# Performance work log

Measured on AMD Instinct MI355X. Metric: run time of the kernel, lower is better.

## Reference

```python
import jax, jax.numpy as jnp
import numpy as np

IN_DIM = 128
OUT_DIM = 128
NUM_HEADS = 8
HEAD_DIM = OUT_DIM // NUM_HEADS  # 16
FFN_DIM = OUT_DIM * 2
LN_EPS = 1e-5


def _layer_norm(x, g, b):
    mu = jnp.mean(x, axis=-1, keepdims=True)
    var = jnp.var(x, axis=-1, keepdims=True)
    return (x - mu) * jax.lax.rsqrt(var + LN_EPS) * g + b


def setup_inputs() -> dict:
    key = jax.random.key(0)
    ks = jax.random.split(key, 12)
    B, N = 4, 2048
    s_in = 1.0 / np.sqrt(IN_DIM)
    s_out = 1.0 / np.sqrt(OUT_DIM)
    s_ffn = 1.0 / np.sqrt(FFN_DIM)
    return {
        "adj_matrix": jax.random.randint(ks[0], (N, N), 0, 2, dtype=jnp.int32),
        "h": jax.random.normal(ks[1], (B, N, IN_DIM), dtype=jnp.float32),
        # Q/K/V: Linear(in_dim, out_dim) with use_bias=False, stored as [in, out]
        "Wq": jax.random.uniform(ks[2], (IN_DIM, OUT_DIM), jnp.float32, -s_in, s_in),
        "Wk": jax.random.uniform(ks[3], (IN_DIM, OUT_DIM), jnp.float32, -s_in, s_in),
        "Wv": jax.random.uniform(ks[4], (IN_DIM, OUT_DIM), jnp.float32, -s_in, s_in),
        "Wo": jax.random.uniform(ks[5], (OUT_DIM, OUT_DIM), jnp.float32, -s_out, s_out),
        "bo": jnp.zeros((OUT_DIM,), jnp.float32),
        "ln1_g": jnp.ones((OUT_DIM,), jnp.float32),
        "ln1_b": jnp.zeros((OUT_DIM,), jnp.float32),
        "W1": jax.random.uniform(ks[6], (OUT_DIM, FFN_DIM), jnp.float32, -s_out, s_out),
        "b1": jnp.zeros((FFN_DIM,), jnp.float32),
        "W2": jax.random.uniform(ks[7], (FFN_DIM, OUT_DIM), jnp.float32, -s_ffn, s_ffn),
        "b2": jnp.zeros((OUT_DIM,), jnp.float32),
        "ln2_g": jnp.ones((OUT_DIM,), jnp.float32),
        "ln2_b": jnp.zeros((OUT_DIM,), jnp.float32),
    }


def reference(adj_matrix, h, Wq, Wk, Wv, Wo, bo, ln1_g, ln1_b,
              W1, b1, W2, b2, ln2_g, ln2_b):
    B, N, _ = h.shape
    # QKV projections -> [B, N, H, D]
    Q = (h @ Wq).reshape(B, N, NUM_HEADS, HEAD_DIM)
    K = (h @ Wk).reshape(B, N, NUM_HEADS, HEAD_DIM)
    V = (h @ Wv).reshape(B, N, NUM_HEADS, HEAD_DIM)
    scores = jnp.einsum('bnhd,bmhd->bhnm', Q, K) / jnp.sqrt(
        jnp.asarray(HEAD_DIM, jnp.float32))
    # adjacency-masked attention: mask broadcast over batch and heads
    mask = (adj_matrix == 0)[None, None, :, :]  # [1,1,N,N]
    scores = jnp.where(mask, -jnp.inf, scores)
    attn = jax.nn.softmax(scores, axis=-1)
    attn_out = jnp.einsum('bhnm,bmhd->bnhd', attn, V).reshape(B, N, OUT_DIM)
    # output projection + residual + LN
    x = h + (attn_out @ Wo + bo)
    x = _layer_norm(x, ln1_g, ln1_b)
    # FFN + residual + LN
    y = jax.nn.relu(x @ W1 + b1) @ W2 + b2
    x = _layer_norm(x + y, ln2_g, ln2_b)
    return x
```

## Files before the change

kernel.cpp:

```cpp
#include <hip/hip_runtime.h>

#define B_   4
#define N_   2048
#define DIM  128
#define NH   8
#define HD   16
#define FFN_ 256
#define LN_EPS 1e-5f
#define BN   (B_*N_)
#define LOG2E 1.44269504f

#if __has_builtin(__builtin_amdgcn_exp2f)
#define EXP2(x) __builtin_amdgcn_exp2f(x)
#else
#define EXP2(x) exp2f(x)
#endif

typedef __bf16 bf16x8 __attribute__((ext_vector_type(8)));
typedef short  s16x8  __attribute__((ext_vector_type(8)));
typedef float  f32x16 __attribute__((ext_vector_type(16)));
typedef unsigned int u32x4 __attribute__((ext_vector_type(4)));

template<class T> struct as_short_vec { using type = s16x8; };

template <class T>
__device__ auto mfma_try(T a, T b, f32x16 c, int)
    -> decltype(__builtin_amdgcn_mfma_f32_32x32x16_bf16(a, b, c, 0, 0, 0)) {
  return __builtin_amdgcn_mfma_f32_32x32x16_bf16(a, b, c, 0, 0, 0);
}
template <class T>
__device__ f32x16 mfma_try(T a, T b, f32x16 c, long) {
  return __builtin_amdgcn_mfma_f32_32x32x16_bf16(
      __builtin_bit_cast(typename as_short_vec<T>::type, a),
      __builtin_bit_cast(typename as_short_vec<T>::type, b), c, 0, 0, 0);
}
__device__ __forceinline__ f32x16 mfma_bf(bf16x8 a, bf16x8 b, f32x16 c) {
  return mfma_try(a, b, c, 0);
}

__global__ __launch_bounds__(256) void k_prep(
    const int* __restrict__ adj,
    const float* __restrict__ W1, const float* __restrict__ W2,
    const float* __restrict__ Wq, const float* __restrict__ Wk,
    const float* __restrict__ Wv, const float* __restrict__ Wo,
    unsigned int* __restrict__ adjbT,
    __bf16* __restrict__ W1t, __bf16* __restrict__ W2t,
    __bf16* __restrict__ Wqt, __bf16* __restrict__ Wkt,
    __bf16* __restrict__ Wvt, __bf16* __restrict__ Wot,
    __bf16* __restrict__ onesb) {
    const int blk = blockIdx.x;
    const int tid = threadIdx.x;
    if (blk < 16384) {
        long long idx = (long long)blk * 256 + tid;
        int v = adj[idx] != 0;
        unsigned long long m = __ballot(v);
        if ((tid & 63) == 0) {
            int q  = (int)(idx >> 11);
            int kc = ((int)idx & 2047) >> 5;
            adjbT[(size_t)kc * 2048 + q]       = (unsigned)m;
            adjbT[(size_t)(kc + 1) * 2048 + q] = (unsigned)(m >> 32);
        }
    } else {
        const int g = (blk - 16384) * 256 + tid;
        {
            int k = g >> 8, n = g & 255;
            W1t[(size_t)n * 128 + k] = (__bf16)W1[(size_t)k * 256 + n];
        }
        {
            int k = g >> 7, n = g & 127;
            W2t[(size_t)n * 256 + k] = (__bf16)W2[(size_t)k * 128 + n];
        }
        if (g < 16384) {
            int k = g >> 7, n = g & 127;
            size_t s = (size_t)k * 128 + n, d = (size_t)n * 128 + k;
            Wqt[d] = (__bf16)(Wq[s] * (0.25f * LOG2E));
            Wkt[d] = (__bf16)Wk[s];
            Wvt[d] = (__bf16)Wv[s];
            Wot[d] = (__bf16)Wo[s];
        }
        if (g < 2080) onesb[g] = (__bf16)1.0f;
    }
}

__global__ __launch_bounds__(768) void k_qkv(
    const float* __restrict__ h,
    const __bf16* __restrict__ Wqt, const __bf16* __restrict__ Wkt,
    const __bf16* __restrict__ Wvt,
    __bf16* __restrict__ Qb, __bf16* __restrict__ Kb, __bf16* __restrict__ Vt) {
    const int r0   = blockIdx.x * 32;
    const int tid  = threadIdx.x;
    const int w    = tid >> 6;
    const int mat  = w >> 2;
    const int ct   = w & 3;
    const int lane = tid & 63;
    const int l31  = lane & 31, hi = lane >> 5;

    __shared__ __bf16 Hs[32 * 128];

    if (tid < 512) {
        int row = tid >> 4, u = tid & 15;
        const float* src = h + (size_t)(r0 + row) * DIM + u * 8;
        float4 f0 = *(const float4*)src, f1 = *(const float4*)(src + 4);
        bf16x8 v;
        v[0] = (__bf16)f0.x; v[1] = (__bf16)f0.y; v[2] = (__bf16)f0.z; v[3] = (__bf16)f0.w;
        v[4] = (__bf16)f1.x; v[5] = (__bf16)f1.y; v[6] = (__bf16)f1.z; v[7] = (__bf16)f1.w;
        int byte = (row * 256 + u * 16) ^ ((row & 7) << 4);
        *(bf16x8*)((char*)Hs + byte) = v;
    }
    __syncthreads();

    const __bf16* Wsel = (mat == 0) ? Wqt : ((mat == 1) ? Wkt : Wvt);

    f32x16 a;
    #pragma unroll
    for (int i = 0; i < 16; ++i) a[i] = 0.f;
    #pragma unroll
    for (int kk = 0; kk < 8; ++kk) {
        int byte = (l31 * 256 + kk * 32 + hi * 16) ^ ((l31 & 7) << 4);
        bf16x8 af = *(const bf16x8*)((const char*)Hs + byte);
        a = mfma_bf(af, *(const bf16x8*)(Wsel + (size_t)(ct * 32 + l31) * 128 + kk * 16 + hi * 8), a);
    }

    const int n  = ct * 32 + l31;
    const int hh = n >> 4, d = n & 15;
    const int b  = r0 >> 11;
    const int nloc0 = r0 & (N_ - 1);
    if (mat < 2) {
        __bf16* dst = (mat == 0) ? Qb : Kb;
        const size_t qbase = (size_t)(b * NH + hh) * N_;
        #pragma unroll
        for (int r = 0; r < 16; ++r) {
            int mm = (r & 3) + 8 * (r >> 2) + 4 * hi;
            dst[(qbase + nloc0 + mm) * HD + d] = (__bf16)a[r];
        }
    } else {
        const size_t vbase = ((size_t)(b * NH + hh) * HD + d) * N_;
        #pragma unroll
        for (int r = 0; r < 16; ++r) {
            int mm   = (r & 3) + 8 * (r >> 2) + 4 * hi;
            int nloc = nloc0 + mm;
            int gg = (nloc >> 2) & 7;
            int ng = (gg & 4) | ((gg & 1) << 1) | ((gg >> 1) & 1);
            Vt[vbase + ((nloc & ~31) | (ng << 2) | (nloc & 3))] = (__bf16)a[r];
        }
    }
}

__global__ __launch_bounds__(512, 4) void k_attn(
    const __bf16* __restrict__ Qb, const __bf16* __restrict__ Kb,
    const __bf16* __restrict__ Vt, const unsigned int* __restrict__ adjbT,
    const __bf16* __restrict__ onesb,
    __bf16* __restrict__ AOb) {
    const int bid  = (blockIdx.x & 7) * 256 + (blockIdx.x >> 3);
    const int qt   = bid & 63;
    const int hh   = (bid >> 6) & 7;
    const int b    = bid >> 9;
    const int kq   = threadIdx.x >> 6;
    const int lane = threadIdx.x & 63;
    const int l31  = lane & 31, hi = lane >> 5;
    const int q     = qt * 32 + l31;
    const int kbase = kq * 256;
    const int NT    = 8;

    __shared__ float accL[7][64][9];
    __shared__ uint2 lutM[16];

    if (threadIdx.x < 16) {
        unsigned v = threadIdx.x;
        lutM[v].x = ((v & 1u) ? 0xFFFFu : 0u) | ((v & 2u) ? 0xFFFF0000u : 0u);
        lutM[v].y = ((v & 4u) ? 0xFFFFu : 0u) | ((v & 8u) ? 0xFFFF0000u : 0u);
    }
    __syncthreads();

    const __bf16* Qh = Qb + (size_t)(b * NH + hh) * N_ * HD;
    const __bf16* Kp = Kb + (size_t)(b * NH + hh) * N_ * HD
                          + (size_t)(kbase + l31) * HD + hi * 8;
    const __bf16* Vp = ((l31 < 16)
        ? (Vt + ((size_t)(b * NH + hh) * HD + l31) * N_)
        : onesb) + kbase + hi * 8;
    const unsigned int* wp = adjbT + (size_t)(kq * NT) * 2048 + q;

    bf16x8 qf = *(const bf16x8*)(Qh + (size_t)q * HD + hi * 8);

    f32x16 acc;
    #pragma unroll
    for (int i = 0; i < 16; ++i) acc[i] = 0.f;
    const f32x16 z = {};

    bf16x8 kf  = *(const bf16x8*)Kp;
    bf16x8 vfa = *(const bf16x8*)Vp;
    bf16x8 vfb = *(const bf16x8*)(Vp + 16);
    unsigned int w32 = wp[0];

    #pragma unroll
    for (int t = 0; t < NT; ++t) {
        bf16x8 kf_n = {}, vfa_n = {}, vfb_n = {};
        unsigned int w32_n = 0;
        if (t + 1 < NT) {
            kf_n  = *(const bf16x8*)(Kp + (t + 1) * 32 * HD);
            vfa_n = *(const bf16x8*)(Vp + (t + 1) * 32);
            vfb_n = *(const bf16x8*)(Vp + (t + 1) * 32 + 16);
            w32_n = wp[(size_t)(t + 1) * 2048];
        }

        const unsigned ws = w32 >> (4 * hi);
        uint2 e0 = lutM[ws & 15u];
        uint2 e1 = lutM[(ws >> 8) & 15u];
        uint2 e2 = lutM[(ws >> 16) & 15u];
        uint2 e3 = lutM[(ws >> 24) & 15u];

        f32x16 st = mfma_bf(kf, qf, z);

        float p[16];
        #pragma unroll
        for (int r = 0; r < 16; ++r) p[r] = EXP2(st[r]);
        bf16x8 pa, pb;
        #pragma unroll
        for (int r = 0; r < 8; ++r) { pa[r] = (__bf16)p[r]; pb[r] = (__bf16)p[r + 8]; }

        u32x4 mA = {e0.x, e0.y, e1.x, e1.y};
        u32x4 mB = {e2.x, e2.y, e3.x, e3.y};
        pa = __builtin_bit_cast(bf16x8, __builtin_bit_cast(u32x4, pa) & mA);
        pb = __builtin_bit_cast(bf16x8, __builtin_bit_cast(u32x4, pb) & mB);

        acc = mfma_bf(vfa, pa, acc);
        acc = mfma_bf(vfb, pb, acc);

        if (t + 1 < NT) { kf = kf_n; vfa = vfa_n; vfb = vfb_n; w32 = w32_n; }
    }

    if (kq != 0) {
        #pragma unroll
        for (int r = 0; r < 9; ++r) accL[kq - 1][lane][r] = acc[r];
    }
    __syncthreads();
    if (kq == 0) {
        float tot[9];
        #pragma unroll
        for (int r = 0; r < 9; ++r) {
            float v = acc[r];
            #pragma unroll
            for (int i = 0; i < 7; ++i) v += accL[i][lane][r];
            tot[r] = v;
        }
        float inv = 1.f / tot[8];
        bf16x8 ov;
        #pragma unroll
        for (int r = 0; r < 8; ++r) ov[r] = (__bf16)(tot[r] * inv);
        u32x4 ou = __builtin_bit_cast(u32x4, ov);
        __bf16* op = AOb + ((size_t)(b * N_ + q)) * DIM + hh * HD + 4 * hi;
        uint2 w0 = { ou[0], ou[1] }, w1 = { ou[2], ou[3] };
        *(uint2*)op       = w0;
        *(uint2*)(op + 8) = w1;
    }
}

__global__ __launch_bounds__(512) void k_tail(
    const __bf16* __restrict__ AOb, const float* __restrict__ h,
    const __bf16* __restrict__ Wot, const float* __restrict__ bo,
    const float* __restrict__ g1, const float* __restrict__ b1ln,
    const __bf16* __restrict__ W1t, const float* __restrict__ b1,
    const __bf16* __restrict__ W2t, const float* __restrict__ b2,
    const float* __restrict__ g2, const float* __restrict__ b2ln,
    float* __restrict__ out) {
    const int r0   = blockIdx.x * 32;
    const int tid  = threadIdx.x;
    const int w    = tid >> 6;
    const int ct   = w & 3;
    const int kh   = w >> 2;
    const int lane = tid & 63;
    const int l31  = lane & 31, hi = lane >> 5;

    __shared__ __bf16 As[32 * 128];
    __shared__ __bf16 Xs[32 * 128];
    __shared__ __bf16 Ts[32 * 256];
    __shared__ float  vv[32][DIM];
    __shared__ float  accT[4][64][16];

    {
        int row = tid >> 4, u = tid & 15;
        bf16x8 v = *(const bf16x8*)(AOb + (size_t)(r0 + row) * DIM + u * 8);
        int byte = (row * 256 + u * 16) ^ ((row & 7) << 4);
        *(bf16x8*)((char*)As + byte) = v;
    }
    __syncthreads();

    f32x16 acc;
    #pragma unroll
    for (int i = 0; i < 16; ++i) acc[i] = 0.f;
    #pragma unroll
    for (int kk = 0; kk < 4; ++kk) {
        int kkk = kh * 4 + kk;
        int byte = (l31 * 256 + kkk * 32 + hi * 16) ^ ((l31 & 7) << 4);
        bf16x8 a = *(const bf16x8*)((const char*)As + byte);
        acc = mfma_bf(a, *(const bf16x8*)(Wot + (size_t)(ct * 32 + l31) * 128 + kkk * 16 + hi * 8), acc);
    }
    if (kh == 1) {
        #pragma unroll
        for (int r = 0; r < 16; ++r) accT[ct][lane][r] = acc[r];
    }
    __syncthreads();
    if (kh == 0) {
        int n = ct * 32 + l31;
        float bb = bo[n];
        #pragma unroll
        for (int r = 0; r < 16; ++r) {
            int mm = (r & 3) + 8 * (r >> 2) + 4 * hi;
            vv[mm][n] = acc[r] + accT[ct][lane][r] + bb + h[(size_t)(r0 + mm) * DIM + n];
        }
    }
    __syncthreads();

    {
        const int ln = lane;
        float gc0 = g1[ln], bc0 = b1ln[ln], gc1 = g1[ln + 64], bc1 = b1ln[ln + 64];
        #pragma unroll
        for (int i = 0; i < 4; ++i) {
            int rr = w * 4 + i;
            float x0 = vv[rr][ln], x1 = vv[rr][ln + 64];
            float s = x0 + x1, s2 = x0 * x0 + x1 * x1;
            for (int off = 1; off < 64; off <<= 1) {
                s  += __shfl_xor(s,  off);
                s2 += __shfl_xor(s2, off);
            }
            float mu  = s * (1.f / DIM);
            float var = s2 * (1.f / DIM) - mu * mu;
            float rs  = rsqrtf(var + LN_EPS);
            int byte0 = (rr * 256 + ln * 2) ^ ((rr & 7) << 4);
            int byte1 = (rr * 256 + (ln + 64) * 2) ^ ((rr & 7) << 4);
            *(__bf16*)((char*)Xs + byte0) = (__bf16)((x0 - mu) * rs * gc0 + bc0);
            *(__bf16*)((char*)Xs + byte1) = (__bf16)((x1 - mu) * rs * gc1 + bc1);
        }
    }
    __syncthreads();

    f32x16 acc1;
    #pragma unroll
    for (int i = 0; i < 16; ++i) acc1[i] = 0.f;
    #pragma unroll
    for (int kk = 0; kk < 8; ++kk) {
        int byte = (l31 * 256 + kk * 32 + hi * 16) ^ ((l31 & 7) << 4);
        bf16x8 a = *(const bf16x8*)((const char*)Xs + byte);
        acc1 = mfma_bf(a, *(const bf16x8*)(W1t + (size_t)(w * 32 + l31) * 128 + kk * 16 + hi * 8), acc1);
    }
    {
        int n = w * 32 + l31;
        float bb = b1[n];
        #pragma unroll
        for (int r = 0; r < 16; ++r) {
            int mm = (r & 3) + 8 * (r >> 2) + 4 * hi;
            float v = fmaxf(acc1[r] + bb, 0.f);
            int byte = (mm * 512 + n * 2) ^ ((mm & 7) << 4);
            *(__bf16*)((char*)Ts + byte) = (__bf16)v;
        }
    }
    __syncthreads();

    f32x16 acc2;
    #pragma unroll
    for (int i = 0; i < 16; ++i) acc2[i] = 0.f;
    #pragma unroll
    for (int kk = 0; kk < 8; ++kk) {
        int kkk = kh * 8 + kk;
        int byte = (l31 * 512 + kkk * 32 + hi * 16) ^ ((l31 & 7) << 4);
        bf16x8 a = *(const bf16x8*)((const char*)Ts + byte);
        acc2 = mfma_bf(a, *(const bf16x8*)(W2t + (size_t)(ct * 32 + l31) * 256 + kkk * 16 + hi * 8), acc2);
    }
    if (kh == 1) {
        #pragma unroll
        for (int r = 0; r < 16; ++r) accT[ct][lane][r] = acc2[r];
    }
    __syncthreads();
    if (kh == 0) {
        int n = ct * 32 + l31;
        float bb = b2[n];
        #pragma unroll
        for (int r = 0; r < 16; ++r) {
            int mm = (r & 3) + 8 * (r >> 2) + 4 * hi;
            int byteR = (mm * 256 + n * 2) ^ ((mm & 7) << 4);
            float resid = (float)*(const __bf16*)((const char*)Xs + byteR);
            vv[mm][n] = acc2[r] + accT[ct][lane][r] + bb + resid;
        }
    }
    __syncthreads();

    {
        const int ln = lane;
        float gc0 = g2[ln], bc0 = b2ln[ln], gc1 = g2[ln + 64], bc1 = b2ln[ln + 64];
        #pragma unroll
        for (int i = 0; i < 4; ++i) {
            int rr = w * 4 + i;
            float x0 = vv[rr][ln], x1 = vv[rr][ln + 64];
            float s = x0 + x1, s2 = x0 * x0 + x1 * x1;
            for (int off = 1; off < 64; off <<= 1) {
                s  += __shfl_xor(s,  off);
                s2 += __shfl_xor(s2, off);
            }
            float mu  = s * (1.f / DIM);
            float var = s2 * (1.f / DIM) - mu * mu;
            float rs  = rsqrtf(var + LN_EPS);
            size_t o = (size_t)(r0 + rr) * DIM;
            out[o + ln]      = (x0 - mu) * rs * gc0 + bc0;
            out[o + ln + 64] = (x1 - mu) * rs * gc1 + bc1;
        }
    }
}

extern "C" void kernel_launch(void* const* d_in, const int* in_sizes, int n_in,
                              void* d_out, int out_size, void* d_ws, size_t ws_size,
                              hipStream_t stream) {
    const int*   adj = (const int*)  d_in[0];
    const float* h   = (const float*)d_in[1];
    const float* Wq  = (const float*)d_in[2];
    const float* Wk  = (const float*)d_in[3];
    const float* Wv  = (const float*)d_in[4];
    const float* Wo  = (const float*)d_in[5];
    const float* bo  = (const float*)d_in[6];
    const float* g1  = (const float*)d_in[7];
    const float* b1l = (const float*)d_in[8];
    const float* W1  = (const float*)d_in[9];
    const float* b1  = (const float*)d_in[10];
    const float* W2  = (const float*)d_in[11];
    const float* b2  = (const float*)d_in[12];
    const float* g2  = (const float*)d_in[13];
    const float* b2l = (const float*)d_in[14];
    float* out = (float*)d_out;

    __bf16* AOb = (__bf16*)d_ws;
    unsigned int* adjbT = (unsigned int*)(AOb + (size_t)BN * DIM);
    __bf16* Qb  = (__bf16*)(adjbT + (size_t)64 * 2048);
    __bf16* Kb  = Qb + (size_t)BN * DIM;
    __bf16* Vt  = Kb + (size_t)BN * DIM;
    __bf16* W1t = Vt + (size_t)BN * DIM;
    __bf16* W2t = W1t + (size_t)DIM * FFN_;
    __bf16* Wqt = W2t + (size_t)DIM * FFN_;
    __bf16* Wkt = Wqt + (size_t)DIM * DIM;
    __bf16* Wvt = Wkt + (size_t)DIM * DIM;
    __bf16* Wot = Wvt + (size_t)DIM * DIM;
    __bf16* onesb = Wot + (size_t)DIM * DIM;

    hipLaunchKernelGGL(k_prep, dim3(16384 + 128), dim3(256), 0, stream,
                       adj, W1, W2, Wq, Wk, Wv, Wo,
                       adjbT, W1t, W2t, Wqt, Wkt, Wvt, Wot, onesb);
    hipLaunchKernelGGL(k_qkv, dim3(BN / 32), dim3(768), 0, stream,
                       h, Wqt, Wkt, Wvt, Qb, Kb, Vt);
    hipLaunchKernelGGL(k_attn, dim3(B_ * NH * (N_ / 32)), dim3(512), 0, stream,
                       Qb, Kb, Vt, adjbT, onesb, AOb);
    hipLaunchKernelGGL(k_tail, dim3(BN / 32), dim3(512), 0, stream,
                       AOb, h, Wot, bo, g1, b1l, W1t, b1, W2t, b2, g2, b2l, out);
}
```

Baseline: 58.12 us.

## Merge prep and QKV kernels into one front kernel with direct weight loads

Combines the adjacency bit-packing, weight casting and QKV projection into a single launch. QKV blocks now read the fp32 Wq/Wk/Wv straight from global memory, converting and scaling them into registers, so the separate transposed bf16 Wq/Wk/Wv buffers and their dependency on a prior kernel go away. The goal is to drop one kernel launch and boundary and let the QKV GEMM overlap with the adjacency packing. In exchange, every QKV block redundantly performs strided fp32 weight loads, and the 768-thread block shape is reused for the adjacency work.

```diff
diff --git a/kernel.cpp b/kernel.cpp
--- a/kernel.cpp
+++ b/kernel.cpp
@@ -38,110 +38,117 @@
   return mfma_try(a, b, c, 0);
 }
 
-__global__ __launch_bounds__(256) void k_prep(
-    const int* __restrict__ adj,
+#define NQKV 256
+#define NADJ 5462
+#define NWCAST 43
+
+__global__ __launch_bounds__(768) void k_front(
+    const int* __restrict__ adj, const float* __restrict__ h,
+    const float* __restrict__ Wq, const float* __restrict__ Wk,
+    const float* __restrict__ Wv,
     const float* __restrict__ W1, const float* __restrict__ W2,
-    const float* __restrict__ Wq, const float* __restrict__ Wk,
-    const float* __restrict__ Wv, const float* __restrict__ Wo,
+    const float* __restrict__ Wo,
+    __bf16* __restrict__ Qb, __bf16* __restrict__ Kb, __bf16* __restrict__ Vt,
     unsigned int* __restrict__ adjbT,
     __bf16* __restrict__ W1t, __bf16* __restrict__ W2t,
-    __bf16* __restrict__ Wqt, __bf16* __restrict__ Wkt,
-    __bf16* __restrict__ Wvt, __bf16* __restrict__ Wot,
-    __bf16* __restrict__ onesb) {
+    __bf16* __restrict__ Wot, __bf16* __restrict__ onesb) {
     const int blk = blockIdx.x;
     const int tid = threadIdx.x;
-    if (blk < 16384) {
-        long long idx = (long long)blk * 256 + tid;
-        int v = adj[idx] != 0;
-        unsigned long long m = __ballot(v);
-        if ((tid & 63) == 0) {
-            int q  = (int)(idx >> 11);
-            int kc = ((int)idx & 2047) >> 5;
-            adjbT[(size_t)kc * 2048 + q]       = (unsigned)m;
-            adjbT[(size_t)(kc + 1) * 2048 + q] = (unsigned)(m >> 32);
+
+    if (blk < NQKV) {
+        const int r0   = blk * 32;
+        const int w    = tid >> 6;
+        const int mat  = w >> 2;
+        const int ct   = w & 3;
+        const int lane = tid & 63;
+        const int l31  = lane & 31, hi = lane >> 5;
+
+        __shared__ __bf16 Hs[32 * 128];
+
+        const float* Wsrc = (mat == 0) ? Wq : ((mat == 1) ? Wk : Wv);
+        const float scale = (mat == 0) ? 0.25f * LOG2E : 1.0f;
+        bf16x8 wf[8];
+        #pragma unroll
+        for (int kk = 0; kk < 8; ++kk) {
+            const int kb = kk * 16 + hi * 8;
+            #pragma unroll
+            for (int j = 0; j < 8; ++j)
+                wf[kk][j] = (__bf16)(Wsrc[(size_t)(kb + j) * 128 + ct * 32 + l31] * scale);
+        }
+
+        if (tid < 512) {
+            int row = tid >> 4, u = tid & 15;
+            const float* src = h + (size_t)(r0 + row) * DIM + u * 8;
+            float4 f0 = *(const float4*)src, f1 = *(const float4*)(src + 4);
+            bf16x8 v;
+            v[0] = (__bf16)f0.x; v[1] = (__bf16)f0.y; v[2] = (__bf16)f0.z; v[3] = (__bf16)f0.w;
+            v[4] = (__bf16)f1.x; v[5] = (__bf16)f1.y; v[6] = (__bf16)f1.z; v[7] = (__bf16)f1.w;
+            int byte = (row * 256 + u * 16) ^ ((row & 7) << 4);
+            *(bf16x8*)((char*)Hs + byte) = v;
+        }
+        __syncthreads();
+
+        f32x16 a;
+        #pragma unroll
+        for (int i = 0; i < 16; ++i) a[i] = 0.f;
+        #pragma unroll
+        for (int kk = 0; kk < 8; ++kk) {
+            int byte = (l31 * 256 + kk * 32 + hi * 16) ^ ((l31 & 7) << 4);
+            bf16x8 af = *(const bf16x8*)((const char*)Hs + byte);
+            a = mfma_bf(af, wf[kk], a);
+        }
+
+        const int n  = ct * 32 + l31;
+        const int hh = n >> 4, d = n & 15;
+        const int b  = r0 >> 11;
+        const int nloc0 = r0 & (N_ - 1);
+        if (mat < 2) {
+            __bf16* dst = (mat == 0) ? Qb : Kb;
+            const size_t qbase = (size_t)(b * NH + hh) * N_;
+            #pragma unroll
+            for (int r = 0; r < 16; ++r) {
+                int mm = (r & 3) + 8 * (r >> 2) + 4 * hi;
+                dst[(qbase + nloc0 + mm) * HD + d] = (__bf16)a[r];
+            }
+        } else {
+            const size_t vbase = ((size_t)(b * NH + hh) * HD + d) * N_;
+            #pragma unroll
+            for (int r = 0; r < 16; ++r) {
+                int mm   = (r & 3) + 8 * (r >> 2) + 4 * hi;
+                int nloc = nloc0 + mm;
+                int gg = (nloc >> 2) & 7;
+                int ng = (gg & 4) | ((gg & 1) << 1) | ((gg >> 1) & 1);
+                Vt[vbase + ((nloc & ~31) | (ng << 2) | (nloc & 3))] = (__bf16)a[r];
+            }
+        }
+    } else if (blk < NQKV + NADJ) {
+        long long idx = (long long)(blk - NQKV) * 768 + tid;
+        if (idx < (long long)N_ * N_) {
+            int v = adj[idx] != 0;
+            unsigned long long m = __ballot(v);
+            if ((tid & 63) == 0) {
+                int q  = (int)(idx >> 11);
+                int kc = ((int)idx & 2047) >> 5;
+                adjbT[(size_t)kc * 2048 + q]       = (unsigned)m;
+                adjbT[(size_t)(kc + 1) * 2048 + q] = (unsigned)(m >> 32);
+            }
         }
     } else {
-        const int g = (blk - 16384) * 256 + tid;
-        {
-            int k = g >> 8, n = g & 255;
-            W1t[(size_t)n * 128 + k] = (__bf16)W1[(size_t)k * 256 + n];
-        }
-        {
-            int k = g >> 7, n = g & 127;
-            W2t[(size_t)n * 256 + k] = (__bf16)W2[(size_t)k * 128 + n];
-        }
-        if (g < 16384) {
-            int k = g >> 7, n = g & 127;
-            size_t s = (size_t)k * 128 + n, d = (size_t)n * 128 + k;
-            Wqt[d] = (__bf16)(Wq[s] * (0.25f * LOG2E));
-            Wkt[d] = (__bf16)Wk[s];
-            Wvt[d] = (__bf16)Wv[s];
-            Wot[d] = (__bf16)Wo[s];
-        }
-        if (g < 2080) onesb[g] = (__bf16)1.0f;
-    }
-}
-
-__global__ __launch_bounds__(768) void k_qkv(
-    const float* __restrict__ h,
-    const __bf16* __restrict__ Wqt, const __bf16* __restrict__ Wkt,
-    const __bf16* __restrict__ Wvt,
-    __bf16* __restrict__ Qb, __bf16* __restrict__ Kb, __bf16* __restrict__ Vt) {
-    const int r0   = blockIdx.x * 32;
-    const int tid  = threadIdx.x;
-    const int w    = tid >> 6;
-    const int mat  = w >> 2;
-    const int ct   = w & 3;
-    const int lane = tid & 63;
-    const int l31  = lane & 31, hi = lane >> 5;
-
-    __shared__ __bf16 Hs[32 * 128];
-
-    if (tid < 512) {
-        int row = tid >> 4, u = tid & 15;
-        const float* src = h + (size_t)(r0 + row) * DIM + u * 8;
-        float4 f0 = *(const float4*)src, f1 = *(const float4*)(src + 4);
-        bf16x8 v;
-        v[0] = (__bf16)f0.x; v[1] = (__bf16)f0.y; v[2] = (__bf16)f0.z; v[3] = (__bf16)f0.w;
-        v[4] = (__bf16)f1.x; v[5] = (__bf16)f1.y; v[6] = (__bf16)f1.z; v[7] = (__bf16)f1.w;
-        int byte = (row * 256 + u * 16) ^ ((row & 7) << 4);
-        *(bf16x8*)((char*)Hs + byte) = v;
-    }
-    __syncthreads();
-
-    const __bf16* Wsel = (mat == 0) ? Wqt : ((mat == 1) ? Wkt : Wvt);
-
-    f32x16 a;
-    #pragma unroll
-    for (int i = 0; i < 16; ++i) a[i] = 0.f;
-    #pragma unroll
-    for (int kk = 0; kk < 8; ++kk) {
-        int byte = (l31 * 256 + kk * 32 + hi * 16) ^ ((l31 & 7) << 4);
-        bf16x8 af = *(const bf16x8*)((const char*)Hs + byte);
-        a = mfma_bf(af, *(const bf16x8*)(Wsel + (size_t)(ct * 32 + l31) * 128 + kk * 16 + hi * 8), a);
-    }
-
-    const int n  = ct * 32 + l31;
-    const int hh = n >> 4, d = n & 15;
-    const int b  = r0 >> 11;
-    const int nloc0 = r0 & (N_ - 1);
-    if (mat < 2) {
-        __bf16* dst = (mat == 0) ? Qb : Kb;
-        const size_t qbase = (size_t)(b * NH + hh) * N_;
-        #pragma unroll
-        for (int r = 0; r < 16; ++r) {
-            int mm = (r & 3) + 8 * (r >> 2) + 4 * hi;
-            dst[(qbase + nloc0 + mm) * HD + d] = (__bf16)a[r];
-        }
-    } else {
-        const size_t vbase = ((size_t)(b * NH + hh) * HD + d) * N_;
-        #pragma unroll
-        for (int r = 0; r < 16; ++r) {
-            int mm   = (r & 3) + 8 * (r >> 2) + 4 * hi;
-            int nloc = nloc0 + mm;
-            int gg = (nloc >> 2) & 7;
-            int ng = (gg & 4) | ((gg & 1) << 1) | ((gg >> 1) & 1);
-            Vt[vbase + ((nloc & ~31) | (ng << 2) | (nloc & 3))] = (__bf16)a[r];
+        const int g = (blk - NQKV - NADJ) * 768 + tid;
+        if (g < 32768) {
+            {
+                int k = g >> 8, n = g & 255;
+                W1t[(size_t)n * 128 + k] = (__bf16)W1[(size_t)k * 256 + n];
+            }
+            {
+                int k = g >> 7, n = g & 127;
+                W2t[(size_t)n * 256 + k] = (__bf16)W2[(size_t)k * 128 + n];
+            }
+            if (g < 16384) {
+                int k = g >> 7, n = g & 127;
+                Wot[(size_t)n * 128 + k] = (__bf16)Wo[(size_t)k * 128 + n];
+            }
+            if (g < 2080) onesb[g] = (__bf16)1.0f;
         }
     }
 }
@@ -433,17 +440,12 @@
     __bf16* Vt  = Kb + (size_t)BN * DIM;
     __bf16* W1t = Vt + (size_t)BN * DIM;
     __bf16* W2t = W1t + (size_t)DIM * FFN_;
-    __bf16* Wqt = W2t + (size_t)DIM * FFN_;
-    __bf16* Wkt = Wqt + (size_t)DIM * DIM;
-    __bf16* Wvt = Wkt + (size_t)DIM * DIM;
-    __bf16* Wot = Wvt + (size_t)DIM * DIM;
+    __bf16* Wot = W2t + (size_t)DIM * FFN_;
     __bf16* onesb = Wot + (size_t)DIM * DIM;
 
-    hipLaunchKernelGGL(k_prep, dim3(16384 + 128), dim3(256), 0, stream,
-                       adj, W1, W2, Wq, Wk, Wv, Wo,
-                       adjbT, W1t, W2t, Wqt, Wkt, Wvt, Wot, onesb);
-    hipLaunchKernelGGL(k_qkv, dim3(BN / 32), dim3(768), 0, stream,
-                       h, Wqt, Wkt, Wvt, Qb, Kb, Vt);
+    hipLaunchKernelGGL(k_front, dim3(NQKV + NADJ + NWCAST), dim3(768), 0, stream,
+                       adj, h, Wq, Wk, Wv, W1, W2, Wo,
+                       Qb, Kb, Vt, adjbT, W1t, W2t, Wot, onesb);
     hipLaunchKernelGGL(k_attn, dim3(B_ * NH * (N_ / 32)), dim3(512), 0, stream,
                        Qb, Kb, Vt, adjbT, onesb, AOb);
     hipLaunchKernelGGL(k_tail, dim3(BN / 32), dim3(512), 0, stream,
```

Measured after the change: 63.11 us. 1.09x slower.

## Process two query tiles per attention block to reuse K/V fragment loads

Applied to the files above, without the earlier changes.

Each attention block now handles 64 queries (two 32-query MFMA tiles) instead of 32, so every K and V fragment loaded from memory feeds both tiles and the grid shrinks by half. The aim is to cut repeated K/V global traffic and per-block overhead such as LUT setup and the cross-wave reduction. In exchange each thread holds twice the accumulators and more live registers, the shared reduction buffer doubles, and there are fewer blocks to spread across CUs.

```diff
diff --git a/kernel.cpp b/kernel.cpp
--- a/kernel.cpp
+++ b/kernel.cpp
@@ -151,18 +151,19 @@
     const __bf16* __restrict__ Vt, const unsigned int* __restrict__ adjbT,
     const __bf16* __restrict__ onesb,
     __bf16* __restrict__ AOb) {
-    const int bid  = (blockIdx.x & 7) * 256 + (blockIdx.x >> 3);
-    const int qt   = bid & 63;
-    const int hh   = (bid >> 6) & 7;
-    const int b    = bid >> 9;
+    const int bid  = (blockIdx.x & 7) * 128 + (blockIdx.x >> 3);
+    const int qt   = bid & 31;
+    const int hh   = (bid >> 5) & 7;
+    const int b    = bid >> 8;
     const int kq   = threadIdx.x >> 6;
     const int lane = threadIdx.x & 63;
     const int l31  = lane & 31, hi = lane >> 5;
-    const int q     = qt * 32 + l31;
+    const int q0    = qt * 64 + l31;
+    const int q1    = q0 + 32;
     const int kbase = kq * 256;
     const int NT    = 8;
 
-    __shared__ float accL[7][64][9];
+    __shared__ float accL[7][64][18];
     __shared__ uint2 lutM[16];
 
     if (threadIdx.x < 16) {
@@ -178,80 +179,112 @@
     const __bf16* Vp = ((l31 < 16)
         ? (Vt + ((size_t)(b * NH + hh) * HD + l31) * N_)
         : onesb) + kbase + hi * 8;
-    const unsigned int* wp = adjbT + (size_t)(kq * NT) * 2048 + q;
-
-    bf16x8 qf = *(const bf16x8*)(Qh + (size_t)q * HD + hi * 8);
-
-    f32x16 acc;
-    #pragma unroll
-    for (int i = 0; i < 16; ++i) acc[i] = 0.f;
+    const unsigned int* wp0 = adjbT + (size_t)(kq * NT) * 2048 + q0;
+    const unsigned int* wp1 = wp0 + 32;
+
+    bf16x8 qf0 = *(const bf16x8*)(Qh + (size_t)q0 * HD + hi * 8);
+    bf16x8 qf1 = *(const bf16x8*)(Qh + (size_t)q1 * HD + hi * 8);
+
+    f32x16 acc0, acc1;
+    #pragma unroll
+    for (int i = 0; i < 16; ++i) { acc0[i] = 0.f; acc1[i] = 0.f; }
     const f32x16 z = {};
 
     bf16x8 kf  = *(const bf16x8*)Kp;
     bf16x8 vfa = *(const bf16x8*)Vp;
     bf16x8 vfb = *(const bf16x8*)(Vp + 16);
-    unsigned int w32 = wp[0];
+    unsigned int w0 = wp0[0], w1 = wp1[0];
 
     #pragma unroll
     for (int t = 0; t < NT; ++t) {
         bf16x8 kf_n = {}, vfa_n = {}, vfb_n = {};
-        unsigned int w32_n = 0;
+        unsigned int w0_n = 0, w1_n = 0;
         if (t + 1 < NT) {
             kf_n  = *(const bf16x8*)(Kp + (t + 1) * 32 * HD);
             vfa_n = *(const bf16x8*)(Vp + (t + 1) * 32);
             vfb_n = *(const bf16x8*)(Vp + (t + 1) * 32 + 16);
-            w32_n = wp[(size_t)(t + 1) * 2048];
-        }
-
-        const unsigned ws = w32 >> (4 * hi);
-        uint2 e0 = lutM[ws & 15u];
-        uint2 e1 = lutM[(ws >> 8) & 15u];
-        uint2 e2 = lutM[(ws >> 16) & 15u];
-        uint2 e3 = lutM[(ws >> 24) & 15u];
-
-        f32x16 st = mfma_bf(kf, qf, z);
-
-        float p[16];
-        #pragma unroll
-        for (int r = 0; r < 16; ++r) p[r] = EXP2(st[r]);
-        bf16x8 pa, pb;
-        #pragma unroll
-        for (int r = 0; r < 8; ++r) { pa[r] = (__bf16)p[r]; pb[r] = (__bf16)p[r + 8]; }
-
-        u32x4 mA = {e0.x, e0.y, e1.x, e1.y};
-        u32x4 mB = {e2.x, e2.y, e3.x, e3.y};
-        pa = __builtin_bit_cast(bf16x8, __builtin_bit_cast(u32x4, pa) & mA);
-        pb = __builtin_bit_cast(bf16x8, __builtin_bit_cast(u32x4, pb) & mB);
-
-        acc = mfma_bf(vfa, pa, acc);
-        acc = mfma_bf(vfb, pb, acc);
-
-        if (t + 1 < NT) { kf = kf_n; vfa = vfa_n; vfb = vfb_n; w32 = w32_n; }
+            w0_n  = wp0[(size_t)(t + 1) * 2048];
+            w1_n  = wp1[(size_t)(t + 1) * 2048];
+        }
+
+        const unsigned ws0 = w0 >> (4 * hi);
+        const unsigned ws1 = w1 >> (4 * hi);
+        uint2 a0 = lutM[ws0 & 15u];
+        uint2 a1 = lutM[(ws0 >> 8) & 15u];
+        uint2 a2 = lutM[(ws0 >> 16) & 15u];
+        uint2 a3 = lutM[(ws0 >> 24) & 15u];
+        uint2 b0 = lutM[ws1 & 15u];
+        uint2 b1 = lutM[(ws1 >> 8) & 15u];
+        uint2 b2 = lutM[(ws1 >> 16) & 15u];
+        uint2 b3 = lutM[(ws1 >> 24) & 15u];
+
+        f32x16 st0 = mfma_bf(kf, qf0, z);
+        f32x16 st1 = mfma_bf(kf, qf1, z);
+
+        float p0[16], p1[16];
+        #pragma unroll
+        for (int r = 0; r < 16; ++r) { p0[r] = EXP2(st0[r]); p1[r] = EXP2(st1[r]); }
+        bf16x8 pa0, pb0, pa1, pb1;
+        #pragma unroll
+        for (int r = 0; r < 8; ++r) {
+            pa0[r] = (__bf16)p0[r]; pb0[r] = (__bf16)p0[r + 8];
+            pa1[r] = (__bf16)p1[r]; pb1[r] = (__bf16)p1[r + 8];
+        }
+
+        u32x4 mA0 = {a0.x, a0.y, a1.x, a1.y};
+        u32x4 mB0 = {a2.x, a2.y, a3.x, a3.y};
+        u32x4 mA1 = {b0.x, b0.y, b1.x, b1.y};
+        u32x4 mB1 = {b2.x, b2.y, b3.x, b3.y};
+        pa0 = __builtin_bit_cast(bf16x8, __builtin_bit_cast(u32x4, pa0) & mA0);
+        pb0 = __builtin_bit_cast(bf16x8, __builtin_bit_cast(u32x4, pb0) & mB0);
+        pa1 = __builtin_bit_cast(bf16x8, __builtin_bit_cast(u32x4, pa1) & mA1);
+        pb1 = __builtin_bit_cast(bf16x8, __builtin_bit_cast(u32x4, pb1) & mB1);
+
+        acc0 = mfma_bf(vfa, pa0, acc0);
+        acc0 = mfma_bf(vfb, pb0, acc0);
+        acc1 = mfma_bf(vfa, pa1, acc1);
+        acc1 = mfma_bf(vfb, pb1, acc1);
+
+        if (t + 1 < NT) { kf = kf_n; vfa = vfa_n; vfb = vfb_n; w0 = w0_n; w1 = w1_n; }
     }
 
     if (kq != 0) {
         #pragma unroll
-        for (int r = 0; r < 9; ++r) accL[kq - 1][lane][r] = acc[r];
+        for (int r = 0; r < 9; ++r) {
+            accL[kq - 1][lane][r]     = acc0[r];
+            accL[kq - 1][lane][9 + r] = acc1[r];
+        }
     }
     __syncthreads();
     if (kq == 0) {
-        float tot[9];
+        float tot0[9], tot1[9];
         #pragma unroll
         for (int r = 0; r < 9; ++r) {
-            float v = acc[r];
+            float v0 = acc0[r], v1 = acc1[r];
             #pragma unroll
-            for (int i = 0; i < 7; ++i) v += accL[i][lane][r];
-            tot[r] = v;
-        }
-        float inv = 1.f / tot[8];
-        bf16x8 ov;
-        #pragma unroll
-        for (int r = 0; r < 8; ++r) ov[r] = (__bf16)(tot[r] * inv);
-        u32x4 ou = __builtin_bit_cast(u32x4, ov);
-        __bf16* op = AOb + ((size_t)(b * N_ + q)) * DIM + hh * HD + 4 * hi;
-        uint2 w0 = { ou[0], ou[1] }, w1 = { ou[2], ou[3] };
-        *(uint2*)op       = w0;
-        *(uint2*)(op + 8) = w1;
+            for (int i = 0; i < 7; ++i) {
+                v0 += accL[i][lane][r];
+                v1 += accL[i][lane][9 + r];
+            }
+            tot0[r] = v0; tot1[r] = v1;
+        }
+        float inv0 = 1.f / tot0[8], inv1 = 1.f / tot1[8];
+        bf16x8 ov0, ov1;
+        #pragma unroll
+        for (int r = 0; r < 8; ++r) {
+            ov0[r] = (__bf16)(tot0[r] * inv0);
+            ov1[r] = (__bf16)(tot1[r] * inv1);
+        }
+        u32x4 ou0 = __builtin_bit_cast(u32x4, ov0);
+        u32x4 ou1 = __builtin_bit_cast(u32x4, ov1);
+        __bf16* op0 = AOb + ((size_t)(b * N_ + q0)) * DIM + hh * HD + 4 * hi;
+        __bf16* op1 = AOb + ((size_t)(b * N_ + q1)) * DIM + hh * HD + 4 * hi;
+        uint2 x0 = { ou0[0], ou0[1] }, x1 = { ou0[2], ou0[3] };
+        uint2 y0 = { ou1[0], ou1[1] }, y1 = { ou1[2], ou1[3] };
+        *(uint2*)op0       = x0;
+        *(uint2*)(op0 + 8) = x1;
+        *(uint2*)op1       = y0;
+        *(uint2*)(op1 + 8) = y1;
     }
 }
 
@@ -444,7 +477,7 @@
                        adjbT, W1t, W2t, Wqt, Wkt, Wvt, Wot, onesb);
     hipLaunchKernelGGL(k_qkv, dim3(BN / 32), dim3(768), 0, stream,
                        h, Wqt, Wkt, Wvt, Qb, Kb, Vt);
-    hipLaunchKernelGGL(k_attn, dim3(B_ * NH * (N_ / 32)), dim3(512), 0, stream,
+    hipLaunchKernelGGL(k_attn, dim3(B_ * NH * (N_ / 64)), dim3(512), 0, stream,
                        Qb, Kb, Vt, adjbT, onesb, AOb);
     hipLaunchKernelGGL(k_tail, dim3(BN / 32), dim3(512), 0, stream,
                        AOb, h, Wot, bo, g1, b1l, W1t, b1, W2t, b2, g2, b2l, out);
```

After: 53.24 us, median of 2. 1.09x faster.

## Process four query tiles per attention block to reuse K/V loads

Applied to the files above, without the earlier changes.

Each attention block now handles 128 queries (four 32-query sub-tiles) instead of 32, so every K and V fragment loaded from memory feeds four score/PV MFMA chains. The grid shrinks by four and the block remap is adjusted to match. The cross-wave reduction buffer grows fourfold and each thread holds four accumulators. The aim is to cut redundant K/V global traffic. In exchange, register pressure and LDS use rise, which may lower occupancy, and there are fewer blocks to spread across CUs. V prefetching into the next iteration is dropped in favour of in-loop loads.

```diff
diff --git a/kernel.cpp b/kernel.cpp
--- a/kernel.cpp
+++ b/kernel.cpp
@@ -151,18 +151,18 @@
     const __bf16* __restrict__ Vt, const unsigned int* __restrict__ adjbT,
     const __bf16* __restrict__ onesb,
     __bf16* __restrict__ AOb) {
-    const int bid  = (blockIdx.x & 7) * 256 + (blockIdx.x >> 3);
-    const int qt   = bid & 63;
-    const int hh   = (bid >> 6) & 7;
-    const int b    = bid >> 9;
+    const int bid  = (blockIdx.x & 7) * 64 + (blockIdx.x >> 3);
+    const int qt   = bid & 15;
+    const int hh   = (bid >> 4) & 7;
+    const int b    = bid >> 7;
     const int kq   = threadIdx.x >> 6;
     const int lane = threadIdx.x & 63;
     const int l31  = lane & 31, hi = lane >> 5;
-    const int q     = qt * 32 + l31;
+    const int qb0   = qt * 128 + l31;
     const int kbase = kq * 256;
     const int NT    = 8;
 
-    __shared__ float accL[7][64][9];
+    __shared__ float accL[7][64][36];
     __shared__ uint2 lutM[16];
 
     if (threadIdx.x < 16) {
@@ -178,80 +178,103 @@
     const __bf16* Vp = ((l31 < 16)
         ? (Vt + ((size_t)(b * NH + hh) * HD + l31) * N_)
         : onesb) + kbase + hi * 8;
-    const unsigned int* wp = adjbT + (size_t)(kq * NT) * 2048 + q;
-
-    bf16x8 qf = *(const bf16x8*)(Qh + (size_t)q * HD + hi * 8);
-
-    f32x16 acc;
-    #pragma unroll
-    for (int i = 0; i < 16; ++i) acc[i] = 0.f;
+    const unsigned int* wp = adjbT + (size_t)(kq * NT) * 2048 + qb0;
+
+    bf16x8 qf[4];
+    #pragma unroll
+    for (int j = 0; j < 4; ++j)
+        qf[j] = *(const bf16x8*)(Qh + (size_t)(qb0 + j * 32) * HD + hi * 8);
+
+    f32x16 acc0, acc1, acc2, acc3;
+    #pragma unroll
+    for (int i = 0; i < 16; ++i) { acc0[i] = 0.f; acc1[i] = 0.f; acc2[i] = 0.f; acc3[i] = 0.f; }
     const f32x16 z = {};
 
-    bf16x8 kf  = *(const bf16x8*)Kp;
-    bf16x8 vfa = *(const bf16x8*)Vp;
-    bf16x8 vfb = *(const bf16x8*)(Vp + 16);
-    unsigned int w32 = wp[0];
+    bf16x8 kf = *(const bf16x8*)Kp;
+    unsigned int w32[4];
+    #pragma unroll
+    for (int j = 0; j < 4; ++j) w32[j] = wp[j * 32];
 
     #pragma unroll
     for (int t = 0; t < NT; ++t) {
-        bf16x8 kf_n = {}, vfa_n = {}, vfb_n = {};
-        unsigned int w32_n = 0;
+        bf16x8 vfa = *(const bf16x8*)(Vp + t * 32);
+        bf16x8 vfb = *(const bf16x8*)(Vp + t * 32 + 16);
+
+        bf16x8 kf_n = {};
+        unsigned int w32_n[4] = {0, 0, 0, 0};
         if (t + 1 < NT) {
-            kf_n  = *(const bf16x8*)(Kp + (t + 1) * 32 * HD);
-            vfa_n = *(const bf16x8*)(Vp + (t + 1) * 32);
-            vfb_n = *(const bf16x8*)(Vp + (t + 1) * 32 + 16);
-            w32_n = wp[(size_t)(t + 1) * 2048];
-        }
-
-        const unsigned ws = w32 >> (4 * hi);
-        uint2 e0 = lutM[ws & 15u];
-        uint2 e1 = lutM[(ws >> 8) & 15u];
-        uint2 e2 = lutM[(ws >> 16) & 15u];
-        uint2 e3 = lutM[(ws >> 24) & 15u];
-
-        f32x16 st = mfma_bf(kf, qf, z);
-
-        float p[16];
-        #pragma unroll
-        for (int r = 0; r < 16; ++r) p[r] = EXP2(st[r]);
-        bf16x8 pa, pb;
-        #pragma unroll
-        for (int r = 0; r < 8; ++r) { pa[r] = (__bf16)p[r]; pb[r] = (__bf16)p[r + 8]; }
-
-        u32x4 mA = {e0.x, e0.y, e1.x, e1.y};
-        u32x4 mB = {e2.x, e2.y, e3.x, e3.y};
-        pa = __builtin_bit_cast(bf16x8, __builtin_bit_cast(u32x4, pa) & mA);
-        pb = __builtin_bit_cast(bf16x8, __builtin_bit_cast(u32x4, pb) & mB);
-
-        acc = mfma_bf(vfa, pa, acc);
-        acc = mfma_bf(vfb, pb, acc);
-
-        if (t + 1 < NT) { kf = kf_n; vfa = vfa_n; vfb = vfb_n; w32 = w32_n; }
+            kf_n = *(const bf16x8*)(Kp + (t + 1) * 32 * HD);
+            #pragma unroll
+            for (int j = 0; j < 4; ++j)
+                w32_n[j] = wp[(size_t)(t + 1) * 2048 + j * 32];
+        }
+
+        #pragma unroll
+        for (int j = 0; j < 4; ++j) {
+            const unsigned ws = w32[j] >> (4 * hi);
+            uint2 e0 = lutM[ws & 15u];
+            uint2 e1 = lutM[(ws >> 8) & 15u];
+            uint2 e2 = lutM[(ws >> 16) & 15u];
+            uint2 e3 = lutM[(ws >> 24) & 15u];
+
+            f32x16 st = mfma_bf(kf, qf[j], z);
+
+            float p[16];
+            #pragma unroll
+            for (int r = 0; r < 16; ++r) p[r] = EXP2(st[r]);
+            bf16x8 pa, pb;
+            #pragma unroll
+            for (int r = 0; r < 8; ++r) { pa[r] = (__bf16)p[r]; pb[r] = (__bf16)p[r + 8]; }
+
+            u32x4 mA = {e0.x, e0.y, e1.x, e1.y};
+            u32x4 mB = {e2.x, e2.y, e3.x, e3.y};
+            pa = __builtin_bit_cast(bf16x8, __builtin_bit_cast(u32x4, pa) & mA);
+            pb = __builtin_bit_cast(bf16x8, __builtin_bit_cast(u32x4, pb) & mB);
+
+            f32x16& acc = (j == 0) ? acc0 : (j == 1) ? acc1 : (j == 2) ? acc2 : acc3;
+            acc = mfma_bf(vfa, pa, acc);
+            acc = mfma_bf(vfb, pb, acc);
+        }
+
+        if (t + 1 < NT) {
+            kf = kf_n;
+            #pragma unroll
+            for (int j = 0; j < 4; ++j) w32[j] = w32_n[j];
+        }
     }
 
     if (kq != 0) {
         #pragma unroll
-        for (int r = 0; r < 9; ++r) accL[kq - 1][lane][r] = acc[r];
+        for (int r = 0; r < 9; ++r) {
+            accL[kq - 1][lane][r]      = acc0[r];
+            accL[kq - 1][lane][9 + r]  = acc1[r];
+            accL[kq - 1][lane][18 + r] = acc2[r];
+            accL[kq - 1][lane][27 + r] = acc3[r];
+        }
     }
     __syncthreads();
     if (kq == 0) {
-        float tot[9];
-        #pragma unroll
-        for (int r = 0; r < 9; ++r) {
-            float v = acc[r];
-            #pragma unroll
-            for (int i = 0; i < 7; ++i) v += accL[i][lane][r];
-            tot[r] = v;
-        }
-        float inv = 1.f / tot[8];
-        bf16x8 ov;
-        #pragma unroll
-        for (int r = 0; r < 8; ++r) ov[r] = (__bf16)(tot[r] * inv);
-        u32x4 ou = __builtin_bit_cast(u32x4, ov);
-        __bf16* op = AOb + ((size_t)(b * N_ + q)) * DIM + hh * HD + 4 * hi;
-        uint2 w0 = { ou[0], ou[1] }, w1 = { ou[2], ou[3] };
-        *(uint2*)op       = w0;
-        *(uint2*)(op + 8) = w1;
+        #pragma unroll
+        for (int j = 0; j < 4; ++j) {
+            const f32x16& accj = (j == 0) ? acc0 : (j == 1) ? acc1 : (j == 2) ? acc2 : acc3;
+            float tot[9];
+            #pragma unroll
+            for (int r = 0; r < 9; ++r) {
+                float v = accj[r];
+                #pragma unroll
+                for (int i = 0; i < 7; ++i) v += accL[i][lane][j * 9 + r];
+                tot[r] = v;
+            }
+            float inv = 1.f / tot[8];
+            bf16x8 ov;
+            #pragma unroll
+            for (int r = 0; r < 8; ++r) ov[r] = (__bf16)(tot[r] * inv);
+            u32x4 ou = __builtin_bit_cast(u32x4, ov);
+            __bf16* op = AOb + ((size_t)(b * N_ + qb0 + j * 32)) * DIM + hh * HD + 4 * hi;
+            uint2 x0 = { ou[0], ou[1] }, x1 = { ou[2], ou[3] };
+            *(uint2*)op       = x0;
+            *(uint2*)(op + 8) = x1;
+        }
     }
 }
 
@@ -444,7 +467,7 @@
                        adjbT, W1t, W2t, Wqt, Wkt, Wvt, Wot, onesb);
     hipLaunchKernelGGL(k_qkv, dim3(BN / 32), dim3(768), 0, stream,
                        h, Wqt, Wkt, Wvt, Qb, Kb, Vt);
-    hipLaunchKernelGGL(k_attn, dim3(B_ * NH * (N_ / 32)), dim3(512), 0, stream,
+    hipLaunchKernelGGL(k_attn, dim3(B_ * NH * (N_ / 128)), dim3(512), 0, stream,
                        Qb, Kb, Vt, adjbT, onesb, AOb);
     hipLaunchKernelGGL(k_tail, dim3(BN / 32), dim3(512), 0, stream,
                        AOb, h, Wot, bo, g1, b1l, W1t, b1, W2t, b2, g2, b2l, out);
```

Measured after the change: 94.84 us. 1.63x slower.
